# Optimization experiments

Measured on AMD Instinct MI355X. Metric: run time of the kernel, lower is better.

The kernel has to match this reference:

```python
import jax, jax.numpy as jnp
import numpy as np

K = 5      # bilateral kernel_size
DIL = 2    # bilateral dilation
HID = 8    # num_hidden_channels


def _conv(x, w, b):
    # 3x3 SAME conv, NCHW / OIHW
    y = jax.lax.conv_general_dilated(x, w, (1, 1), 'SAME',
                                     dimension_numbers=('NCHW', 'OIHW', 'NCHW'))
    return y + b[None, :, None, None]


def _relu(x):
    return jnp.maximum(x, 0)


def _maxpool2(x):
    return jax.lax.reduce_window(x, -jnp.inf, jax.lax.max,
                                 (1, 1, 2, 2), (1, 1, 2, 2), 'VALID')


def _convT_2x2_s2(x, w, b):
    # PyTorch ConvTranspose2d(k=2, s=2), weight (in, out, 2, 2):
    # equivalent to conv with lhs_dilation=2, spatially-flipped transposed kernel, pad 1.
    wk = jnp.flip(jnp.transpose(w, (1, 0, 2, 3)), (2, 3))  # -> (out, in, 2, 2)
    y = jax.lax.conv_general_dilated(x, wk, (1, 1), [(1, 1), (1, 1)],
                                     lhs_dilation=(2, 2),
                                     dimension_numbers=('NCHW', 'OIHW', 'NCHW'))
    return y + b[None, :, None, None]


def _encoder(x, ws, bs, wt, bt):
    # EncoderUNet2
    d = _conv(_relu(_conv(_relu(_conv(x, ws[0], bs[0])), ws[1], bs[1])), ws[2], bs[2])
    e = _maxpool2(d)
    for i in (3, 4, 5):
        e = _relu(_conv(e, ws[i], bs[i]))
    u = _convT_2x2_s2(e, wt, bt) + d
    u = _conv(_relu(_conv(_relu(_conv(u, ws[6], bs[6])), ws[7], bs[7])), ws[8], bs[8])
    return u


def _bilateral(x, params):
    # Learned per-channel color/spatial affinity bilateral filter.
    # weight(p,q) = exp(sum_c params[c]*(x_c(q)-x_c(p))^2 + params[C]*dy^2 + params[C+1]*dx^2)
    # params <= 0 so weights <= 1; zero-padded out-of-bounds taps are masked out.
    B, C, H, W = x.shape
    half = K // 2
    r = half * DIL
    xp = jnp.pad(x, ((0, 0), (0, 0), (r, r), (r, r)))
    mp = jnp.pad(jnp.ones((B, 1, H, W), x.dtype), ((0, 0), (0, 0), (r, r), (r, r)))
    cw = params[:C]
    sy = params[C]
    sx = params[C + 1]
    num = jnp.zeros_like(x)
    den = jnp.zeros((B, 1, H, W), x.dtype)
    for dy in range(-half, half + 1):
        for dx in range(-half, half + 1):
            oy, ox = dy * DIL, dx * DIL
            sh = xp[:, :, r + oy:r + oy + H, r + ox:r + ox + W]
            m = mp[:, :, r + oy:r + oy + H, r + ox:r + ox + W]
            logw = jnp.einsum('bchw,c->bhw', (sh - x) ** 2, cw) + sy * (oy * oy) + sx * (ox * ox)
            w = jnp.exp(logw)[:, None, :, :] * m
            num = num + w * sh
            den = den + w
    return num / den  # center tap has weight 1, so den >= 1


def _forward(x, ws, bs, wt, bt, fparams):
    feats = _encoder(x, ws, bs, wt, bt)
    combined = jnp.concatenate([x[:, :3 + HID], feats], axis=1)  # (B, 27, H, W)
    filt = _bilateral(combined, fparams)
    return filt[:, :3 + HID]  # dynamic_size = hidden + 3 = 11


def setup_inputs() -> dict:
    key = jax.random.key(0)
    ks = jax.random.split(key, 24)
    def rn(k, shape, s=0.1):
        return s * jax.random.normal(k, shape, dtype=jnp.float32)
    d = {'x': jax.random.normal(ks[0], (4, 16, 512, 512), dtype=jnp.float32)}
    shapes = [(16, 16, 3, 3), (16, 16, 3, 3), (32, 16, 3, 3),
              (32, 32, 3, 3), (32, 32, 3, 3), (32, 32, 3, 3),
              (16, 32, 3, 3), (16, 16, 3, 3), (16, 16, 3, 3)]
    for i, s in enumerate(shapes):
        d[f'w{i}'] = rn(ks[1 + i], s)
        d[f'b{i}'] = rn(ks[10 + i], (s[0],), 0.01)
    d['wt'] = rn(ks[19], (32, 32, 2, 2))  # ConvTranspose2d weight (in, out, kh, kw)
    d['bt'] = rn(ks[20], (32,), 0.01)
    # params init: randn().abs().mul(-0.01), clamped <= 0
    d['fparams'] = -0.01 * jnp.abs(jax.random.normal(ks[21], (29,), dtype=jnp.float32))
    return d


def reference(x, w0, w1, w2, w3, w4, w5, w6, w7, w8,
              b0, b1, b2, b3, b4, b5, b6, b7, b8, wt, bt, fparams):
    ws = (w0, w1, w2, w3, w4, w5, w6, w7, w8)
    bs = (b0, b1, b2, b3, b4, b5, b6, b7, b8)
    return _forward(x, ws, bs, wt, bt, fparams)
```

## Files before the change

kernel.cpp:

```cpp
#include <hip/hip_runtime.h>
#include <cstdint>
#include <cstddef>

typedef _Float16 f16;
typedef __attribute__((ext_vector_type(8))) _Float16 f16x8;
typedef __attribute__((ext_vector_type(2))) _Float16 f16x2;
typedef __attribute__((ext_vector_type(4))) float f32x4;

#if defined(__has_builtin)
#if __has_builtin(__builtin_amdgcn_fdot2)
#define HAS_FDOT2 1
#endif
#endif

__device__ __forceinline__ float hu2f(unsigned int u16) {
    f16 h; unsigned short s = (unsigned short)u16;
    __builtin_memcpy(&h, &s, 2); return (float)h;
}
__device__ __forceinline__ unsigned short f2hu(float f) {
    f16 h = (f16)f;
    unsigned short u; __builtin_memcpy(&u, &h, 2); return u;
}
__device__ __forceinline__ void unpk8(const uint4 u, float* f) {
    f[0] = hu2f(u.x & 0xffffu); f[1] = hu2f(u.x >> 16);
    f[2] = hu2f(u.y & 0xffffu); f[3] = hu2f(u.y >> 16);
    f[4] = hu2f(u.z & 0xffffu); f[5] = hu2f(u.z >> 16);
    f[6] = hu2f(u.w & 0xffffu); f[7] = hu2f(u.w >> 16);
}
__device__ __forceinline__ unsigned int packh2(float a, float b) {
    return (unsigned int)f2hu(a) | ((unsigned int)f2hu(b) << 16);
}
__device__ __forceinline__ float dotacc(unsigned int gh, unsigned int q, float acc) {
#ifdef HAS_FDOT2
    f16x2 a, b;
    __builtin_memcpy(&a, &gh, 4);
    __builtin_memcpy(&b, &q, 4);
    return __builtin_amdgcn_fdot2(a, b, acc, false);
#else
    return fmaf(hu2f(gh & 0xffffu), hu2f(q & 0xffffu),
                fmaf(hu2f(gh >> 16), hu2f(q >> 16), acc));
#endif
}

struct WSrc { const float* w[10]; };

__global__ __launch_bounds__(256) void prep_k(WSrc src, f16* __restrict__ wp,
                                              f16* __restrict__ wpT) {
    const int l = blockIdx.x;
    if (l == 9) {
        const float* wt = src.w[9];
        for (int e = threadIdx.x; e < 4096; e += 256) {
            const int j = e & 7;
            const int lane = (e >> 3) & 63;
            const int mt = e >> 9;
            const int m = mt * 16 + (lane & 15);
            const int k = ((lane >> 4) << 3) + j;
            wpT[e] = (f16)wt[k * 128 + m];
        }
        return;
    }
    const int CI[9]  = {16, 16, 16, 32, 32, 32, 32, 16, 16};
    const int CO[9]  = {16, 16, 32, 32, 32, 32, 16, 16, 16};
    const int OFF[9] = {0, 3072, 6144, 12288, 21504, 30720, 39936, 44544, 47616};
    const int cin = CI[l], cout = CO[l], nct = cout / 16;
    const int nt = (cin == 32) ? 9 : 6;
    const int sz = nt * nct * 512;
    const float* w = src.w[l];
    f16* dst = wp + OFF[l];
    for (int e = threadIdx.x; e < sz; e += 256) {
        const int j = e & 7;
        const int lane = (e >> 3) & 63;
        const int r = e >> 9;
        const int ct = r % nct, tp = r / nct;
        const int co = ct * 16 + (lane & 15);
        const int kk = ((lane >> 4) << 3) + j;
        float v;
        if (cin == 32) {
            const int ci = kk, ky = tp / 3, kx = tp % 3;
            v = w[((co * 32 + ci) * 3 + ky) * 3 + kx];
        } else {
            const int ci = kk & 15, dxs = kk >> 4;
            const int ky = tp >> 1, kx = (tp & 1) * 2 + dxs;
            v = (kx < 3) ? w[((co * 16 + ci) * 3 + ky) * 3 + kx] : 0.0f;
        }
        dst[e] = (f16)v;
    }
}

__global__ __launch_bounds__(256) void xtonhwc_k(
    const float* __restrict__ x, f16* __restrict__ xh)
{
    const int idx = blockIdx.x * 256 + threadIdx.x;
    const int n = idx >> 18, px = idx & 262143;
    const float* xp = x + (size_t)n * 16 * 262144 + px;
    unsigned short r[16];
    #pragma unroll
    for (int c = 0; c < 16; ++c) r[c] = f2hu(xp[(size_t)c * 262144]);
    __builtin_memcpy(xh + (size_t)idx * 16, r, 32);
}

template<int CIN, int COUT, bool RELU>
__global__ __launch_bounds__(256) void convm2_k(
    const f16* __restrict__ in, const f16* __restrict__ wp,
    const float* __restrict__ bias, f16* __restrict__ out)
{
    constexpr int Wd = 512;
    constexpr int PLANE = Wd * Wd;
    constexpr int NCT = COUT / 16;
    constexpr int NT = (CIN == 32) ? 9 : 6;
    constexpr int CB = CIN * 2;

    const int lane = threadIdx.x & 63;
    const int l4 = lane >> 4;
    const int lm = lane & 15;
    const int wv = threadIdx.x >> 6;
    const int n = blockIdx.y;
    const int y0 = (blockIdx.x >> 1) * 2;
    const int xw = (blockIdx.x & 1) * 256 + wv * 64;

    f16x8 afr[NT][NCT];
    #pragma unroll
    for (int tp = 0; tp < NT; ++tp)
        #pragma unroll
        for (int ct = 0; ct < NCT; ++ct)
            __builtin_memcpy(&afr[tp][ct],
                wp + ((size_t)(tp * NCT + ct) * 64 + lane) * 8, 16);

    f32x4 acc[2][4][NCT];
    #pragma unroll
    for (int ct = 0; ct < NCT; ++ct) {
        const float4 bv = *reinterpret_cast<const float4*>(bias + ct * 16 + l4 * 4);
        #pragma unroll
        for (int o = 0; o < 2; ++o)
            #pragma unroll
            for (int t = 0; t < 4; ++t) {
                acc[o][t][ct][0] = bv.x; acc[o][t][ct][1] = bv.y;
                acc[o][t][ct][2] = bv.z; acc[o][t][ct][3] = bv.w;
            }
    }

    bool okL[4], okR[4];
    #pragma unroll
    for (int t = 0; t < 4; ++t) {
        const int xl = xw + t * 16 + lm;
        okL[t] = (xl != 0)      || (CIN == 16 && lane >= 32);
        okR[t] = (xl != Wd - 1) || (CIN == 16 && lane >= 32);
    }

    int laneoff;
    if (CIN == 32) laneoff = lm * 64 + l4 * 16;
    else           laneoff = lm * 32 + (l4 >> 1) * 32 + (l4 & 1) * 16;

    const char* base = (const char*)in
        + ((size_t)n * PLANE + (size_t)y0 * Wd + xw) * CB + laneoff;

    #pragma unroll
    for (int r = 0; r < 4; ++r) {
        const int ry = y0 - 1 + r;
        if ((unsigned)ry >= (unsigned)Wd) continue;
        const char* rb = base + (r - 1) * Wd * CB;
        if (CIN == 32) {
            #pragma unroll
            for (int dx = 0; dx < 3; ++dx)
                #pragma unroll
                for (int t = 0; t < 4; ++t) {
                    uint4 u = *reinterpret_cast<const uint4*>(rb + ((dx - 1) + t * 16) * 64);
                    if (dx == 0 && !okL[t]) { u.x = 0; u.y = 0; u.z = 0; u.w = 0; }
                    if (dx == 2 && !okR[t]) { u.x = 0; u.y = 0; u.z = 0; u.w = 0; }
                    f16x8 b; __builtin_memcpy(&b, &u, 16);
                    if (r <= 2)
                        #pragma unroll
                        for (int ct = 0; ct < NCT; ++ct)
                            acc[0][t][ct] = __builtin_amdgcn_mfma_f32_16x16x32_f16(
                                afr[r * 3 + dx][ct], b, acc[0][t][ct], 0, 0, 0);
                    if (r >= 1)
                        #pragma unroll
                        for (int ct = 0; ct < NCT; ++ct)
                            acc[1][t][ct] = __builtin_amdgcn_mfma_f32_16x16x32_f16(
                                afr[(r - 1) * 3 + dx][ct], b, acc[1][t][ct], 0, 0, 0);
                }
        } else {
            #pragma unroll
            for (int p = 0; p < 2; ++p)
                #pragma unroll
                for (int t = 0; t < 4; ++t) {
                    uint4 u = *reinterpret_cast<const uint4*>(rb + (p ? 32 : -32) + t * 512);
                    if (p == 0 && !okL[t]) { u.x = 0; u.y = 0; u.z = 0; u.w = 0; }
                    if (p == 1 && !okR[t]) { u.x = 0; u.y = 0; u.z = 0; u.w = 0; }
                    f16x8 b; __builtin_memcpy(&b, &u, 16);
                    if (r <= 2)
                        #pragma unroll
                        for (int ct = 0; ct < NCT; ++ct)
                            acc[0][t][ct] = __builtin_amdgcn_mfma_f32_16x16x32_f16(
                                afr[r * 2 + p][ct], b, acc[0][t][ct], 0, 0, 0);
                    if (r >= 1)
                        #pragma unroll
                        for (int ct = 0; ct < NCT; ++ct)
                            acc[1][t][ct] = __builtin_amdgcn_mfma_f32_16x16x32_f16(
                                afr[(r - 1) * 2 + p][ct], b, acc[1][t][ct], 0, 0, 0);
                }
        }
    }

    #pragma unroll
    for (int o = 0; o < 2; ++o) {
        char* ob = (char*)out
            + ((size_t)n * PLANE + (size_t)(y0 + o) * Wd + xw) * (COUT * 2);
        #pragma unroll
        for (int t = 0; t < 4; ++t)
            #pragma unroll
            for (int ct = 0; ct < NCT; ++ct) {
                float a0 = acc[o][t][ct][0], a1 = acc[o][t][ct][1];
                float a2 = acc[o][t][ct][2], a3 = acc[o][t][ct][3];
                if (RELU) {
                    a0 = fmaxf(a0, 0.f); a1 = fmaxf(a1, 0.f);
                    a2 = fmaxf(a2, 0.f); a3 = fmaxf(a3, 0.f);
                }
                ushort4 pk;
                pk.x = f2hu(a0); pk.y = f2hu(a1); pk.z = f2hu(a2); pk.w = f2hu(a3);
                *reinterpret_cast<ushort4*>(
                    ob + ((size_t)(t * 16 + lm) * COUT + ct * 16 + l4 * 4) * 2) = pk;
            }
    }
}

template<int CIN, int COUT, bool RELU, int LW>
__global__ __launch_bounds__(256) void convm_k(
    const f16* __restrict__ in, const f16* __restrict__ wp,
    const float* __restrict__ bias, f16* __restrict__ out)
{
    constexpr int Wd = 1 << LW;
    constexpr int PLANE = Wd * Wd;
    constexpr int NCT = COUT / 16;
    constexpr int NT = (CIN == 32) ? 9 : 6;
    constexpr int CB = CIN * 2;

    const int lane = threadIdx.x & 63;
    const int l4 = lane >> 4;
    const int lm = lane & 15;
    const int wv = threadIdx.x >> 6;
    const int n = blockIdx.y;
    const int pxb = blockIdx.x * 256 + wv * 64;
    const int y = pxb >> LW;
    const int xw = pxb & (Wd - 1);

    f16x8 afr[NT][NCT];
    #pragma unroll
    for (int tp = 0; tp < NT; ++tp)
        #pragma unroll
        for (int ct = 0; ct < NCT; ++ct)
            __builtin_memcpy(&afr[tp][ct],
                wp + ((size_t)(tp * NCT + ct) * 64 + lane) * 8, 16);

    f32x4 acc[4][NCT];
    #pragma unroll
    for (int ct = 0; ct < NCT; ++ct) {
        const float4 bv = *reinterpret_cast<const float4*>(bias + ct * 16 + l4 * 4);
        #pragma unroll
        for (int t = 0; t < 4; ++t) {
            acc[t][ct][0] = bv.x; acc[t][ct][1] = bv.y;
            acc[t][ct][2] = bv.z; acc[t][ct][3] = bv.w;
        }
    }

    bool okL[4], okR[4];
    #pragma unroll
    for (int t = 0; t < 4; ++t) {
        const int xl = xw + t * 16 + lm;
        okL[t] = (xl != 0)      || (CIN == 16 && lane >= 32);
        okR[t] = (xl != Wd - 1) || (CIN == 16 && lane >= 32);
    }

    int laneoff;
    if (CIN == 32) laneoff = lm * 64 + l4 * 16;
    else           laneoff = lm * 32 + (l4 >> 1) * 32 + (l4 & 1) * 16;

    const char* base = (const char*)in
        + ((size_t)n * PLANE + (size_t)y * Wd + xw) * CB + laneoff;

    #pragma unroll
    for (int ky = 0; ky < 3; ++ky) {
        if ((unsigned)(y + ky - 1) >= (unsigned)Wd) continue;
        const char* rb = base + (ky - 1) * Wd * CB;
        if (CIN == 32) {
            #pragma unroll
            for (int dx = 0; dx < 3; ++dx) {
                #pragma unroll
                for (int t = 0; t < 4; ++t) {
                    uint4 u = *reinterpret_cast<const uint4*>(rb + ((dx - 1) + t * 16) * 64);
                    if (dx == 0 && !okL[t]) { u.x = 0; u.y = 0; u.z = 0; u.w = 0; }
                    if (dx == 2 && !okR[t]) { u.x = 0; u.y = 0; u.z = 0; u.w = 0; }
                    f16x8 b; __builtin_memcpy(&b, &u, 16);
                    #pragma unroll
                    for (int ct = 0; ct < NCT; ++ct)
                        acc[t][ct] = __builtin_amdgcn_mfma_f32_16x16x32_f16(
                            afr[ky * 3 + dx][ct], b, acc[t][ct], 0, 0, 0);
                }
            }
        } else {
            #pragma unroll
            for (int p = 0; p < 2; ++p) {
                #pragma unroll
                for (int t = 0; t < 4; ++t) {
                    uint4 u = *reinterpret_cast<const uint4*>(rb + (p ? 32 : -32) + t * 512);
                    if (p == 0 && !okL[t]) { u.x = 0; u.y = 0; u.z = 0; u.w = 0; }
                    if (p == 1 && !okR[t]) { u.x = 0; u.y = 0; u.z = 0; u.w = 0; }
                    f16x8 b; __builtin_memcpy(&b, &u, 16);
                    #pragma unroll
                    for (int ct = 0; ct < NCT; ++ct)
                        acc[t][ct] = __builtin_amdgcn_mfma_f32_16x16x32_f16(
                            afr[ky * 2 + p][ct], b, acc[t][ct], 0, 0, 0);
                }
            }
        }
    }

    char* ob = (char*)out + ((size_t)n * PLANE + (size_t)y * Wd + xw) * (COUT * 2);
    #pragma unroll
    for (int t = 0; t < 4; ++t)
        #pragma unroll
        for (int ct = 0; ct < NCT; ++ct) {
            float a0 = acc[t][ct][0], a1 = acc[t][ct][1];
            float a2 = acc[t][ct][2], a3 = acc[t][ct][3];
            if (RELU) {
                a0 = fmaxf(a0, 0.f); a1 = fmaxf(a1, 0.f);
                a2 = fmaxf(a2, 0.f); a3 = fmaxf(a3, 0.f);
            }
            ushort4 pk;
            pk.x = f2hu(a0); pk.y = f2hu(a1); pk.z = f2hu(a2); pk.w = f2hu(a3);
            *reinterpret_cast<ushort4*>(
                ob + ((size_t)(t * 16 + lm) * COUT + ct * 16 + l4 * 4) * 2) = pk;
        }
}

__global__ __launch_bounds__(256) void pool_k(
    const f16* __restrict__ in, f16* __restrict__ out)
{
    const int idx = blockIdx.x * 256 + threadIdx.x;
    const int c8 = (idx & 3) * 8;
    const int opx = idx >> 2;
    const int n = opx >> 16;
    const int p = opx & 65535;
    const int oy = p >> 8, ox = p & 255;
    const char* ip = (const char*)in
        + (((size_t)n * 262144 + (size_t)(2 * oy) * 512 + 2 * ox) * 32 + c8) * 2;
    uint4 ua = *reinterpret_cast<const uint4*>(ip);
    uint4 ub = *reinterpret_cast<const uint4*>(ip + 64);
    uint4 uc = *reinterpret_cast<const uint4*>(ip + 512 * 64);
    uint4 ud = *reinterpret_cast<const uint4*>(ip + 512 * 64 + 64);
    float a[8], b[8], c[8], d[8];
    unpk8(ua, a); unpk8(ub, b); unpk8(uc, c); unpk8(ud, d);
    unsigned short r[8];
    #pragma unroll
    for (int k = 0; k < 8; ++k)
        r[k] = f2hu(fmaxf(fmaxf(a[k], b[k]), fmaxf(c[k], d[k])));
    __builtin_memcpy((char*)out + (((size_t)n * 65536 + p) * 32 + c8) * 2, r, 16);
}

__global__ __launch_bounds__(256) void convTm_k(
    const f16* __restrict__ e, const f16* __restrict__ wpT,
    const float* __restrict__ bt, f16* __restrict__ du)
{
    __shared__ float lds[4][16 * 132];
    const int lane = threadIdx.x & 63;
    const int wv = threadIdx.x >> 6;
    const int l4 = lane >> 4, lm = lane & 15;
    const int n = blockIdx.y;
    const int row = blockIdx.x;
    const int j0 = wv * 64;

    f16x8 afr[8];
    #pragma unroll
    for (int mt = 0; mt < 8; ++mt)
        __builtin_memcpy(&afr[mt], wpT + ((size_t)(mt * 64 + lane)) * 8, 16);

    float bco[8];
    #pragma unroll
    for (int mt = 0; mt < 8; ++mt) bco[mt] = bt[mt * 4 + l4];

    const char* ep = (const char*)e + ((size_t)n * 65536 + (size_t)row * 256 + j0) * 64;
    float* L = lds[wv];

    const int ra = lane >> 5;
    const int ru = lane & 31;
    const int rj = ru >> 1;
    const int rb = ru & 1;

    #pragma unroll 1
    for (int nt = 0; nt < 4; ++nt) {
        f16x8 bf;
        __builtin_memcpy(&bf, ep + (nt * 16 + lm) * 64 + l4 * 16, 16);

        #pragma unroll
        for (int mt = 0; mt < 8; ++mt) {
            f32x4 acc;
            acc[0] = bco[mt]; acc[1] = bco[mt]; acc[2] = bco[mt]; acc[3] = bco[mt];
            acc = __builtin_amdgcn_mfma_f32_16x16x32_f16(afr[mt], bf, acc, 0, 0, 0);
            float4 st; st.x = acc[0]; st.y = acc[1]; st.z = acc[2]; st.w = acc[3];
            *reinterpret_cast<float4*>(L + lm * 132 + mt * 16 + l4 * 4) = st;
        }
        __syncthreads();

        {
            const float* Ls = L + rj * 132 + ra * 2 + rb;
            char* dp = (char*)du
                + (((size_t)n * 262144
                    + (size_t)(2 * row + ra) * 512
                    + (size_t)(2 * (j0 + nt * 16 + rj) + rb)) * 32) * 2;
            float add[32];
            #pragma unroll
            for (int co = 0; co < 32; ++co) add[co] = Ls[co * 4];
            #pragma unroll
            for (int q = 0; q < 4; ++q) {
                uint4 u = *reinterpret_cast<const uint4*>(dp + q * 16);
                float dv[8]; unpk8(u, dv);
                unsigned short r[8];
                #pragma unroll
                for (int k = 0; k < 8; ++k) r[k] = f2hu(dv[k] + add[q * 8 + k]);
                __builtin_memcpy(dp + q * 16, r, 16);
            }
        }
        __syncthreads();
    }
}

__global__ __launch_bounds__(256) void sprep_k(
    const float* __restrict__ xin, const f16* __restrict__ feats,
    const float* __restrict__ fp, float* __restrict__ S)
{
    constexpr int PLANE = 512 * 512;
    const int pix = blockIdx.x * 256 + threadIdx.x;
    const int n = blockIdx.y;

    const float* xb = xin + (size_t)n * 16 * PLANE + pix;
    const char* fb = (const char*)feats + ((size_t)n * PLANE + pix) * 32;

    float s = 0.0f;
    #pragma unroll
    for (int i = 0; i < 11; ++i) {
        const float v = xb[(size_t)i * PLANE];
        s = fmaf(fp[i] * v, v, s);
    }
    uint4 u0 = *reinterpret_cast<const uint4*>(fb);
    uint4 u1 = *reinterpret_cast<const uint4*>(fb + 16);
    float fv[16];
    unpk8(u0, fv); unpk8(u1, fv + 8);
    #pragma unroll
    for (int i = 0; i < 16; ++i)
        s = fmaf(fp[11 + i] * fv[i], fv[i], s);

    S[(size_t)n * PLANE + pix] = s;
}

__global__ __launch_bounds__(256) void bil_k(
    const float* __restrict__ xin, const f16* __restrict__ feats,
    const float* __restrict__ Sbuf, const float* __restrict__ fp,
    float* __restrict__ out)
{
    constexpr int PLANE = 512 * 512;
    const int n = blockIdx.y;
    const int rp = blockIdx.x >> 1;
    const int xx = ((blockIdx.x & 1) << 8) + threadIdx.x;
    const int y0 = ((rp >> 1) << 2) + (rp & 1);

    const float sy = fp[27], sx = fp[28];

    const int p0 = y0 * 512 + xx;
    const float* xb = xin + (size_t)n * 16 * PLANE + p0;
    const char* fb = (const char*)feats + ((size_t)n * PLANE + p0) * 32;
    const float* Sb = Sbuf + (size_t)n * PLANE + p0;

    float g0[11], g1[11];
    #pragma unroll
    for (int i = 0; i < 11; ++i) {
        g0[i] = fp[i] * xb[(size_t)i * PLANE];
        g1[i] = fp[i] * xb[(size_t)i * PLANE + 1024];
    }
    unsigned int g0h[8], g1h[8];
    {
        uint4 cu0 = *reinterpret_cast<const uint4*>(fb);
        uint4 cu1 = *reinterpret_cast<const uint4*>(fb + 16);
        const unsigned int* cq = (const unsigned int*)&cu0;
        const unsigned int* cq2 = (const unsigned int*)&cu1;
        #pragma unroll
        for (int j = 0; j < 8; ++j) {
            const unsigned int q = (j < 4) ? cq[j] : cq2[j - 4];
            g0h[j] = packh2(fp[11 + 2 * j] * hu2f(q & 0xffffu),
                            fp[12 + 2 * j] * hu2f(q >> 16));
        }
        cu0 = *reinterpret_cast<const uint4*>(fb + 32768);
        cu1 = *reinterpret_cast<const uint4*>(fb + 32768 + 16);
        #pragma unroll
        for (int j = 0; j < 8; ++j) {
            const unsigned int q = (j < 4) ? ((const unsigned int*)&cu0)[j]
                                           : ((const unsigned int*)&cu1)[j - 4];
            g1h[j] = packh2(fp[11 + 2 * j] * hu2f(q & 0xffffu),
                            fp[12 + 2 * j] * hu2f(q >> 16));
        }
    }
    const float Sp0 = Sb[0];
    const float Sp1 = Sb[1024];

    float num0[11], num1[11];
    #pragma unroll
    for (int i = 0; i < 11; ++i) { num0[i] = 0.f; num1[i] = 0.f; }
    float den0 = 0.f, den1 = 0.f;

    #pragma unroll
    for (int o = -4; o <= 6; o += 2) {
        const int r = y0 + o;
        if ((unsigned)r > 511u) continue;
        const float b0 = fmaf(sy, (float)(o * o), Sp0);
        const float b1 = fmaf(sy, (float)((o - 2) * (o - 2)), Sp1);
        const float* xr = xb + o * 512;
        const char* fr = fb + (ptrdiff_t)o * 512 * 32;
        const float* Sr = Sb + o * 512;
        #pragma unroll
        for (int dx = -2; dx <= 2; ++dx) {
            const int xv = xx + 2 * dx;
            if ((unsigned)xv > 511u) continue;
            const int off = dx * 2;

            float sv[11];
            #pragma unroll
            for (int i = 0; i < 11; ++i) sv[i] = xr[(size_t)i * PLANE + off];
            const uint4 u0 = *reinterpret_cast<const uint4*>(fr + off * 32);
            const uint4 u1 = *reinterpret_cast<const uint4*>(fr + off * 32 + 16);
            const unsigned int* fq = (const unsigned int*)&u0;
            const unsigned int* fq2 = (const unsigned int*)&u1;
            const float Sq = Sr[off] + sx * (float)(4 * dx * dx);

            if (o <= 4) {
                float cr = g0[0] * sv[0];
                #pragma unroll
                for (int i = 1; i < 11; ++i) cr = fmaf(g0[i], sv[i], cr);
                #pragma unroll
                for (int j = 0; j < 8; ++j)
                    cr = dotacc(g0h[j], (j < 4) ? fq[j] : fq2[j - 4], cr);
                const float w = __expf(fmaf(-2.0f, cr, Sq + b0));
                #pragma unroll
                for (int i = 0; i < 11; ++i) num0[i] = fmaf(w, sv[i], num0[i]);
                den0 += w;
            }
            if (o >= -2) {
                float cr = g1[0] * sv[0];
                #pragma unroll
                for (int i = 1; i < 11; ++i) cr = fmaf(g1[i], sv[i], cr);
                #pragma unroll
                for (int j = 0; j < 8; ++j)
                    cr = dotacc(g1h[j], (j < 4) ? fq[j] : fq2[j - 4], cr);
                const float w = __expf(fmaf(-2.0f, cr, Sq + b1));
                #pragma unroll
                for (int i = 0; i < 11; ++i) num1[i] = fmaf(w, sv[i], num1[i]);
                den1 += w;
            }
        }
    }

    const float i0 = 1.f / den0, i1 = 1.f / den1;
    float* ob = out + (size_t)n * 11 * PLANE + p0;
    #pragma unroll
    for (int i = 0; i < 11; ++i) {
        ob[(size_t)i * PLANE] = num0[i] * i0;
        ob[(size_t)i * PLANE + 1024] = num1[i] * i1;
    }
}

extern "C" void kernel_launch(void* const* d_in, const int* in_sizes, int n_in,
                              void* d_out, int out_size, void* d_ws, size_t ws_size,
                              hipStream_t stream)
{
    const float* x = (const float*)d_in[0];
    const float* Wv[9];
    const float* Bv[9];
    if (in_sizes[2] == 16) {
        for (int i = 0; i < 9; ++i) {
            Wv[i] = (const float*)d_in[1 + 2 * i];
            Bv[i] = (const float*)d_in[2 + 2 * i];
        }
    } else {
        for (int i = 0; i < 9; ++i) {
            Wv[i] = (const float*)d_in[1 + i];
            Bv[i] = (const float*)d_in[10 + i];
        }
    }
    const float* wt = (const float*)d_in[19];
    const float* bt = (const float*)d_in[20];
    const float* fp = (const float*)d_in[21];
    float* out = (float*)d_out;

    constexpr size_t MiB = 1ull << 20;
    char* ws = (char*)d_ws;

    f16* wp  = (f16*)(ws + 4096);
    f16* wpT = (f16*)(ws + 256 * 1024);
    f16 *xh, *du, *bufA, *bufB;
    if (ws_size >= 165 * MiB) {
        xh   = (f16*)(ws + 1 * MiB);
        du   = (f16*)(ws + 34 * MiB);
        bufA = (f16*)(ws + 99 * MiB);
        bufB = (f16*)(ws + 132 * MiB);
    } else if (ws_size >= 132 * MiB) {
        xh   = (f16*)(ws + 1 * MiB);
        du   = (f16*)(ws + 34 * MiB);
        bufA = (f16*)(ws + 99 * MiB);
        bufB = xh;
    } else {
        xh   = (f16*)((char*)d_out + 256);
        du   = (f16*)(ws + 1 * MiB);
        bufA = (f16*)(ws + 66 * MiB);
        bufB = xh;
    }
    float* Sbuf = (float*)du;

    WSrc srcs;
    for (int i = 0; i < 9; ++i) srcs.w[i] = Wv[i];
    srcs.w[9] = wt;

    prep_k<<<10, 256, 0, stream>>>(srcs, wp, wpT);
    xtonhwc_k<<<4096, 256, 0, stream>>>(x, xh);

    const dim3 blk(256);
    const dim3 g512(512, 4);
    const dim3 gpix(1024, 4);
    const dim3 g256(256, 4);

    convm2_k<16, 16, true ><<<g512, blk, 0, stream>>>(xh,   wp + 0,     Bv[0], bufA);
    convm2_k<16, 16, true ><<<g512, blk, 0, stream>>>(bufA, wp + 3072,  Bv[1], bufB);
    convm2_k<16, 32, false><<<g512, blk, 0, stream>>>(bufB, wp + 6144,  Bv[2], du);

    pool_k<<<4096, blk, 0, stream>>>(du, bufA);
    convm_k<32, 32, true, 8><<<g256, blk, 0, stream>>>(bufA, wp + 12288, Bv[3], bufB);
    convm_k<32, 32, true, 8><<<g256, blk, 0, stream>>>(bufB, wp + 21504, Bv[4], bufA);
    convm_k<32, 32, true, 8><<<g256, blk, 0, stream>>>(bufA, wp + 30720, Bv[5], bufB);

    convTm_k<<<g256, blk, 0, stream>>>(bufB, wpT, bt, du);

    convm2_k<32, 16, true ><<<g512, blk, 0, stream>>>(du,   wp + 39936, Bv[6], bufA);
    convm2_k<16, 16, true ><<<g512, blk, 0, stream>>>(bufA, wp + 44544, Bv[7], bufB);
    convm2_k<16, 16, false><<<g512, blk, 0, stream>>>(bufB, wp + 47616, Bv[8], bufA);

    sprep_k<<<gpix, blk, 0, stream>>>(x, bufA, fp, Sbuf);
    bil_k<<<dim3(512, 4), blk, 0, stream>>>(x, bufA, Sbuf, fp, out);

    (void)n_in; (void)out_size;
}
```

Measured before the change: 372.7 us.

## Fuse maxpool and bilateral S-prep into conv epilogues, unify conv kernels

Generalizes the two-row convm2_k kernel over width and adds optional epilogues. The third encoder conv now writes the 2x2 max-pooled output directly using lane shuffles, and the last decoder conv computes the per-pixel S term for the bilateral filter. This removes the standalone pool_k and sprep_k launches and their extra passes over the feature maps. The 256-wide convs also switch to the two-row variant with half the blocks. The cost is that the S-prep epilogue runs only on a quarter of lanes and issues strided fp32 reads of x there, which may be poorly coalesced.

```diff
diff --git a/kernel.cpp b/kernel.cpp
--- a/kernel.cpp
+++ b/kernel.cpp
@@ -99,24 +99,27 @@
     __builtin_memcpy(xh + (size_t)idx * 16, r, 32);
 }
 
-template<int CIN, int COUT, bool RELU>
+template<int CIN, int COUT, bool RELU, int LW, bool POOL, bool SPREP>
 __global__ __launch_bounds__(256) void convm2_k(
     const f16* __restrict__ in, const f16* __restrict__ wp,
-    const float* __restrict__ bias, f16* __restrict__ out)
+    const float* __restrict__ bias, f16* __restrict__ out,
+    f16* __restrict__ pout, const float* __restrict__ xin,
+    const float* __restrict__ fp, float* __restrict__ Sbuf)
 {
-    constexpr int Wd = 512;
+    constexpr int Wd = 1 << LW;
     constexpr int PLANE = Wd * Wd;
     constexpr int NCT = COUT / 16;
     constexpr int NT = (CIN == 32) ? 9 : 6;
     constexpr int CB = CIN * 2;
+    constexpr int COLB = Wd / 256;
 
     const int lane = threadIdx.x & 63;
     const int l4 = lane >> 4;
     const int lm = lane & 15;
     const int wv = threadIdx.x >> 6;
     const int n = blockIdx.y;
-    const int y0 = (blockIdx.x >> 1) * 2;
-    const int xw = (blockIdx.x & 1) * 256 + wv * 64;
+    const int y0 = (blockIdx.x / COLB) * 2;
+    const int xw = (blockIdx.x % COLB) * 256 + wv * 64;
 
     f16x8 afr[NT][NCT];
     #pragma unroll
@@ -222,139 +225,62 @@
                     ob + ((size_t)(t * 16 + lm) * COUT + ct * 16 + l4 * 4) * 2) = pk;
             }
     }
-}
-
-template<int CIN, int COUT, bool RELU, int LW>
-__global__ __launch_bounds__(256) void convm_k(
-    const f16* __restrict__ in, const f16* __restrict__ wp,
-    const float* __restrict__ bias, f16* __restrict__ out)
-{
-    constexpr int Wd = 1 << LW;
-    constexpr int PLANE = Wd * Wd;
-    constexpr int NCT = COUT / 16;
-    constexpr int NT = (CIN == 32) ? 9 : 6;
-    constexpr int CB = CIN * 2;
-
-    const int lane = threadIdx.x & 63;
-    const int l4 = lane >> 4;
-    const int lm = lane & 15;
-    const int wv = threadIdx.x >> 6;
-    const int n = blockIdx.y;
-    const int pxb = blockIdx.x * 256 + wv * 64;
-    const int y = pxb >> LW;
-    const int xw = pxb & (Wd - 1);
-
-    f16x8 afr[NT][NCT];
-    #pragma unroll
-    for (int tp = 0; tp < NT; ++tp)
-        #pragma unroll
-        for (int ct = 0; ct < NCT; ++ct)
-            __builtin_memcpy(&afr[tp][ct],
-                wp + ((size_t)(tp * NCT + ct) * 64 + lane) * 8, 16);
-
-    f32x4 acc[4][NCT];
-    #pragma unroll
-    for (int ct = 0; ct < NCT; ++ct) {
-        const float4 bv = *reinterpret_cast<const float4*>(bias + ct * 16 + l4 * 4);
+
+    if constexpr (POOL) {
+        constexpr int HPL = (Wd >> 1) * (Wd >> 1);
         #pragma unroll
         for (int t = 0; t < 4; ++t) {
-            acc[t][ct][0] = bv.x; acc[t][ct][1] = bv.y;
-            acc[t][ct][2] = bv.z; acc[t][ct][3] = bv.w;
-        }
-    }
-
-    bool okL[4], okR[4];
-    #pragma unroll
-    for (int t = 0; t < 4; ++t) {
-        const int xl = xw + t * 16 + lm;
-        okL[t] = (xl != 0)      || (CIN == 16 && lane >= 32);
-        okR[t] = (xl != Wd - 1) || (CIN == 16 && lane >= 32);
-    }
-
-    int laneoff;
-    if (CIN == 32) laneoff = lm * 64 + l4 * 16;
-    else           laneoff = lm * 32 + (l4 >> 1) * 32 + (l4 & 1) * 16;
-
-    const char* base = (const char*)in
-        + ((size_t)n * PLANE + (size_t)y * Wd + xw) * CB + laneoff;
-
-    #pragma unroll
-    for (int ky = 0; ky < 3; ++ky) {
-        if ((unsigned)(y + ky - 1) >= (unsigned)Wd) continue;
-        const char* rb = base + (ky - 1) * Wd * CB;
-        if (CIN == 32) {
-            #pragma unroll
-            for (int dx = 0; dx < 3; ++dx) {
-                #pragma unroll
-                for (int t = 0; t < 4; ++t) {
-                    uint4 u = *reinterpret_cast<const uint4*>(rb + ((dx - 1) + t * 16) * 64);
-                    if (dx == 0 && !okL[t]) { u.x = 0; u.y = 0; u.z = 0; u.w = 0; }
-                    if (dx == 2 && !okR[t]) { u.x = 0; u.y = 0; u.z = 0; u.w = 0; }
-                    f16x8 b; __builtin_memcpy(&b, &u, 16);
+            const int col = xw + t * 16 + lm;
+            #pragma unroll
+            for (int ct = 0; ct < NCT; ++ct) {
+                float m[4];
+                #pragma unroll
+                for (int rg = 0; rg < 4; ++rg) {
+                    m[rg] = fmaxf(acc[0][t][ct][rg], acc[1][t][ct][rg]);
+                    m[rg] = fmaxf(m[rg], __shfl_xor(m[rg], 1));
+                }
+                if ((lm & 1) == 0) {
+                    ushort4 pk;
+                    pk.x = f2hu(m[0]); pk.y = f2hu(m[1]);
+                    pk.z = f2hu(m[2]); pk.w = f2hu(m[3]);
+                    char* pb = (char*)pout
+                        + (((size_t)n * HPL + (size_t)(y0 >> 1) * (Wd >> 1) + (col >> 1))
+                           * COUT + ct * 16 + l4 * 4) * 2;
+                    *reinterpret_cast<ushort4*>(pb) = pk;
+                }
+            }
+        }
+    }
+
+    if constexpr (SPREP) {
+        float fpv[4];
+        #pragma unroll
+        for (int rg = 0; rg < 4; ++rg) fpv[rg] = fp[11 + l4 * 4 + rg];
+        #pragma unroll
+        for (int o = 0; o < 2; ++o) {
+            #pragma unroll
+            for (int t = 0; t < 4; ++t) {
+                float s = 0.f;
+                #pragma unroll
+                for (int rg = 0; rg < 4; ++rg) {
+                    const float v = (float)(f16)acc[o][t][0][rg];
+                    s = fmaf(fpv[rg] * v, v, s);
+                }
+                s += __shfl_xor(s, 16);
+                s += __shfl_xor(s, 32);
+                if (l4 == 0) {
+                    const int px = (y0 + o) * Wd + xw + t * 16 + lm;
+                    const float* xp = xin + (size_t)n * 16 * PLANE + px;
                     #pragma unroll
-                    for (int ct = 0; ct < NCT; ++ct)
-                        acc[t][ct] = __builtin_amdgcn_mfma_f32_16x16x32_f16(
-                            afr[ky * 3 + dx][ct], b, acc[t][ct], 0, 0, 0);
-                }
-            }
-        } else {
-            #pragma unroll
-            for (int p = 0; p < 2; ++p) {
-                #pragma unroll
-                for (int t = 0; t < 4; ++t) {
-                    uint4 u = *reinterpret_cast<const uint4*>(rb + (p ? 32 : -32) + t * 512);
-                    if (p == 0 && !okL[t]) { u.x = 0; u.y = 0; u.z = 0; u.w = 0; }
-                    if (p == 1 && !okR[t]) { u.x = 0; u.y = 0; u.z = 0; u.w = 0; }
-                    f16x8 b; __builtin_memcpy(&b, &u, 16);
-                    #pragma unroll
-                    for (int ct = 0; ct < NCT; ++ct)
-                        acc[t][ct] = __builtin_amdgcn_mfma_f32_16x16x32_f16(
-                            afr[ky * 2 + p][ct], b, acc[t][ct], 0, 0, 0);
-                }
-            }
-        }
-    }
-
-    char* ob = (char*)out + ((size_t)n * PLANE + (size_t)y * Wd + xw) * (COUT * 2);
-    #pragma unroll
-    for (int t = 0; t < 4; ++t)
-        #pragma unroll
-        for (int ct = 0; ct < NCT; ++ct) {
-            float a0 = acc[t][ct][0], a1 = acc[t][ct][1];
-            float a2 = acc[t][ct][2], a3 = acc[t][ct][3];
-            if (RELU) {
-                a0 = fmaxf(a0, 0.f); a1 = fmaxf(a1, 0.f);
-                a2 = fmaxf(a2, 0.f); a3 = fmaxf(a3, 0.f);
-            }
-            ushort4 pk;
-            pk.x = f2hu(a0); pk.y = f2hu(a1); pk.z = f2hu(a2); pk.w = f2hu(a3);
-            *reinterpret_cast<ushort4*>(
-                ob + ((size_t)(t * 16 + lm) * COUT + ct * 16 + l4 * 4) * 2) = pk;
-        }
-}
-
-__global__ __launch_bounds__(256) void pool_k(
-    const f16* __restrict__ in, f16* __restrict__ out)
-{
-    const int idx = blockIdx.x * 256 + threadIdx.x;
-    const int c8 = (idx & 3) * 8;
-    const int opx = idx >> 2;
-    const int n = opx >> 16;
-    const int p = opx & 65535;
-    const int oy = p >> 8, ox = p & 255;
-    const char* ip = (const char*)in
-        + (((size_t)n * 262144 + (size_t)(2 * oy) * 512 + 2 * ox) * 32 + c8) * 2;
-    uint4 ua = *reinterpret_cast<const uint4*>(ip);
-    uint4 ub = *reinterpret_cast<const uint4*>(ip + 64);
-    uint4 uc = *reinterpret_cast<const uint4*>(ip + 512 * 64);
-    uint4 ud = *reinterpret_cast<const uint4*>(ip + 512 * 64 + 64);
-    float a[8], b[8], c[8], d[8];
-    unpk8(ua, a); unpk8(ub, b); unpk8(uc, c); unpk8(ud, d);
-    unsigned short r[8];
-    #pragma unroll
-    for (int k = 0; k < 8; ++k)
-        r[k] = f2hu(fmaxf(fmaxf(a[k], b[k]), fmaxf(c[k], d[k])));
-    __builtin_memcpy((char*)out + (((size_t)n * 65536 + p) * 32 + c8) * 2, r, 16);
+                    for (int i = 0; i < 11; ++i) {
+                        const float v = xp[(size_t)i * PLANE];
+                        s = fmaf(fp[i] * v, v, s);
+                    }
+                    Sbuf[(size_t)n * PLANE + px] = s;
+                }
+            }
+        }
+    }
 }
 
 __global__ __launch_bounds__(256) void convTm_k(
@@ -422,34 +348,6 @@
         }
         __syncthreads();
     }
-}
-
-__global__ __launch_bounds__(256) void sprep_k(
-    const float* __restrict__ xin, const f16* __restrict__ feats,
-    const float* __restrict__ fp, float* __restrict__ S)
-{
-    constexpr int PLANE = 512 * 512;
-    const int pix = blockIdx.x * 256 + threadIdx.x;
-    const int n = blockIdx.y;
-
-    const float* xb = xin + (size_t)n * 16 * PLANE + pix;
-    const char* fb = (const char*)feats + ((size_t)n * PLANE + pix) * 32;
-
-    float s = 0.0f;
-    #pragma unroll
-    for (int i = 0; i < 11; ++i) {
-        const float v = xb[(size_t)i * PLANE];
-        s = fmaf(fp[i] * v, v, s);
-    }
-    uint4 u0 = *reinterpret_cast<const uint4*>(fb);
-    uint4 u1 = *reinterpret_cast<const uint4*>(fb + 16);
-    float fv[16];
-    unpk8(u0, fv); unpk8(u1, fv + 8);
-    #pragma unroll
-    for (int i = 0; i < 16; ++i)
-        s = fmaf(fp[11 + i] * fv[i], fv[i], s);
-
-    S[(size_t)n * PLANE + pix] = s;
 }
 
 __global__ __launch_bounds__(256) void bil_k(
@@ -622,25 +520,32 @@
 
     const dim3 blk(256);
     const dim3 g512(512, 4);
-    const dim3 gpix(1024, 4);
-    const dim3 g256(256, 4);
-
-    convm2_k<16, 16, true ><<<g512, blk, 0, stream>>>(xh,   wp + 0,     Bv[0], bufA);
-    convm2_k<16, 16, true ><<<g512, blk, 0, stream>>>(bufA, wp + 3072,  Bv[1], bufB);
-    convm2_k<16, 32, false><<<g512, blk, 0, stream>>>(bufB, wp + 6144,  Bv[2], du);
-
-    pool_k<<<4096, blk, 0, stream>>>(du, bufA);
-    convm_k<32, 32, true, 8><<<g256, blk, 0, stream>>>(bufA, wp + 12288, Bv[3], bufB);
-    convm_k<32, 32, true, 8><<<g256, blk, 0, stream>>>(bufB, wp + 21504, Bv[4], bufA);
-    convm_k<32, 32, true, 8><<<g256, blk, 0, stream>>>(bufA, wp + 30720, Bv[5], bufB);
-
-    convTm_k<<<g256, blk, 0, stream>>>(bufB, wpT, bt, du);
-
-    convm2_k<32, 16, true ><<<g512, blk, 0, stream>>>(du,   wp + 39936, Bv[6], bufA);
-    convm2_k<16, 16, true ><<<g512, blk, 0, stream>>>(bufA, wp + 44544, Bv[7], bufB);
-    convm2_k<16, 16, false><<<g512, blk, 0, stream>>>(bufB, wp + 47616, Bv[8], bufA);
-
-    sprep_k<<<gpix, blk, 0, stream>>>(x, bufA, fp, Sbuf);
+    const dim3 g256(128, 4);
+    const dim3 gT(256, 4);
+
+    convm2_k<16, 16, true,  9, false, false><<<g512, blk, 0, stream>>>(
+        xh,   wp + 0,     Bv[0], bufA, nullptr, nullptr, nullptr, nullptr);
+    convm2_k<16, 16, true,  9, false, false><<<g512, blk, 0, stream>>>(
+        bufA, wp + 3072,  Bv[1], bufB, nullptr, nullptr, nullptr, nullptr);
+    convm2_k<16, 32, false, 9, true,  false><<<g512, blk, 0, stream>>>(
+        bufB, wp + 6144,  Bv[2], du,   bufA,    nullptr, nullptr, nullptr);
+
+    convm2_k<32, 32, true,  8, false, false><<<g256, blk, 0, stream>>>(
+        bufA, wp + 12288, Bv[3], bufB, nullptr, nullptr, nullptr, nullptr);
+    convm2_k<32, 32, true,  8, false, false><<<g256, blk, 0, stream>>>(
+        bufB, wp + 21504, Bv[4], bufA, nullptr, nullptr, nullptr, nullptr);
+    convm2_k<32, 32, true,  8, false, false><<<g256, blk, 0, stream>>>(
+        bufA, wp + 30720, Bv[5], bufB, nullptr, nullptr, nullptr, nullptr);
+
+    convTm_k<<<gT, blk, 0, stream>>>(bufB, wpT, bt, du);
+
+    convm2_k<32, 16, true,  9, false, false><<<g512, blk, 0, stream>>>(
+        du,   wp + 39936, Bv[6], bufA, nullptr, nullptr, nullptr, nullptr);
+    convm2_k<16, 16, true,  9, false, false><<<g512, blk, 0, stream>>>(
+        bufA, wp + 44544, Bv[7], bufB, nullptr, nullptr, nullptr, nullptr);
+    convm2_k<16, 16, false, 9, false, true ><<<g512, blk, 0, stream>>>(
+        bufB, wp + 47616, Bv[8], bufA, nullptr, x, fp, Sbuf);
+
     bil_k<<<dim3(512, 4), blk, 0, stream>>>(x, bufA, Sbuf, fp, out);
 
     (void)n_in; (void)out_size;
```

New measurement: 341.4 us (median of 2 runs). -8.4%, faster.
